# Performance work log

Hardware: AMD Instinct MI355X
Metric: run time of the kernel (lower is better)

The kernel has to match this reference:

```python
import math
import jax, jax.numpy as jnp
import numpy as np

T = 4096
D_MODEL = 1024
NUM_HEADS = 16
HEAD_DIM = D_MODEL // NUM_HEADS


def setup_inputs() -> dict:
    key = jax.random.key(0)
    k_x, k_wqkv, k_wproj = jax.random.split(key, 3)
    # match eqx.nn.Linear init scale: U(-1/sqrt(in), 1/sqrt(in)); randn*small works too,
    # but keep magnitudes reasonable so softmax isn't saturated.
    s_in = 1.0 / math.sqrt(D_MODEL)
    x = jax.random.normal(k_x, (T, D_MODEL), dtype=jnp.float32)
    W_qkv = jax.random.normal(k_wqkv, (3 * D_MODEL, D_MODEL), dtype=jnp.float32) * s_in
    b_qkv = jnp.zeros((3 * D_MODEL,), dtype=jnp.float32)
    W_proj = jax.random.normal(k_wproj, (D_MODEL, D_MODEL), dtype=jnp.float32) * s_in
    b_proj = jnp.zeros((D_MODEL,), dtype=jnp.float32)
    return {"x": x, "W_qkv": W_qkv, "b_qkv": b_qkv, "W_proj": W_proj, "b_proj": b_proj}


def reference(x, W_qkv, b_qkv, W_proj, b_proj):
    T_, C = x.shape  # (seq, d_model)
    H, hd = NUM_HEADS, HEAD_DIM
    # c_attn: eqx Linear computes W @ x + b per token -> x @ W.T + b
    qkv = x @ W_qkv.T + b_qkv  # (T, 3C)
    q, k, v = jnp.split(qkv, 3, axis=1)
    # (T, C) -> (H, T, hd)
    q = q.reshape(T_, H, hd).swapaxes(0, 1)
    k = k.reshape(T_, H, hd).swapaxes(0, 1)
    v = v.reshape(T_, H, hd).swapaxes(0, 1)
    scores = jnp.einsum("htd,hsd->hts", q, k) / math.sqrt(hd)  # (H, T, T)
    causal = jnp.tril(jnp.ones((T_, T_), dtype=bool))
    scores = jnp.where(causal, scores, -jnp.inf)
    attn = jax.nn.softmax(scores, axis=-1)
    y = jnp.einsum("hts,hsd->htd", attn, v)  # (H, T, hd)
    y = y.swapaxes(0, 1).reshape(T_, C)
    y = y @ W_proj.T + b_proj
    return y
```

## Files before the change

kernel.cpp:

```cpp
#include <hip/hip_runtime.h>
#include <math.h>
#include <string.h>

#define T_SEQ 4096
#define DM 1024
#define NH 16
#define HD 64

typedef short s8v __attribute__((ext_vector_type(8)));
typedef float f4v __attribute__((ext_vector_type(4)));

__device__ inline unsigned short f2bf(float f) {
    unsigned u; memcpy(&u, &f, 4);
    u = u + 0x7fffu + ((u >> 16) & 1u);
    return (unsigned short)(u >> 16);
}

__device__ inline float exp2fn(float x) {
#if __has_builtin(__builtin_amdgcn_exp2f)
    return __builtin_amdgcn_exp2f(x);
#else
    return exp2f(x);
#endif
}

__device__ inline void gld_lds16(const void* g, void* l) {
    __builtin_amdgcn_global_load_lds(
        (const __attribute__((address_space(1))) void*)g,
        (__attribute__((address_space(3))) void*)l, 16, 0, 0);
}

__global__ __launch_bounds__(256)
void cvt3(const float* __restrict__ i0, unsigned short* __restrict__ o0, int n0,
          const float* __restrict__ i1, unsigned short* __restrict__ o1, int n1,
          const float* __restrict__ i2, unsigned short* __restrict__ o2, int n2) {
    int i = blockIdx.x * 256 + threadIdx.x;
    const float* in; unsigned short* out; int j;
    if (i < n0)           { in = i0; out = o0; j = i; }
    else if (i < n0 + n1) { in = i1; out = o1; j = i - n0; }
    else if (i < n0 + n1 + n2) { in = i2; out = o2; j = i - n0 - n1; }
    else return;
    const float4* p = (const float4*)(in + (size_t)j * 8);
    float4 a = p[0], b = p[1];
    unsigned short o[8] = {f2bf(a.x), f2bf(a.y), f2bf(a.z), f2bf(a.w),
                           f2bf(b.x), f2bf(b.y), f2bf(b.z), f2bf(b.w)};
    uint4 pk; memcpy(&pk, o, 16);
    *(uint4*)(out + (size_t)j * 8) = pk;
}

template<int MODE, int TN>
__global__ __launch_bounds__(256)
void gemm_bt_mfma(const unsigned short* __restrict__ A, const unsigned short* __restrict__ B,
                  const float* __restrict__ bias, void* __restrict__ Cout,
                  unsigned short* __restrict__ vT,
                  int M, int N, int K) {
    constexpr int NF = TN / 32;
    __shared__ __align__(16) short As[4096];
    __shared__ __align__(16) short Bs[TN * 32];
    const int tid = threadIdx.x;
    const int w = tid >> 6, lane = tid & 63;
    const int wr = w >> 1, wc = w & 1;
    const int m0 = blockIdx.y * 128, n0 = blockIdx.x * TN;

    const bool doA = (w < 2);
    const bool doStage = doA || ((w & 1) * 64 < TN);
    const unsigned short* src = doA ? A : B;
    const int rbase = (doA ? m0 : n0) + (w & 1) * 64;
    const unsigned short* gsrc = src + (size_t)(rbase + (lane & 15)) * K + ((lane >> 4) * 8);
    short* ldst = (doA ? As : Bs) + ((w & 1) * 4) * 512;

    f4v acc[4][NF];
    #pragma unroll
    for (int i = 0; i < 4; ++i)
        #pragma unroll
        for (int j = 0; j < NF; ++j) acc[i][j] = (f4v){0.f, 0.f, 0.f, 0.f};

    for (int k0 = 0; k0 < K; k0 += 32) {
        __syncthreads();
        if (doStage) {
            #pragma unroll
            for (int i = 0; i < 4; ++i)
                gld_lds16(gsrc + (size_t)(i * 16) * K + k0, ldst + i * 512);
        }
        __syncthreads();

        s8v af[4], bf[NF];
        #pragma unroll
        for (int i = 0; i < 4; ++i) af[i] = *(const s8v*)&As[((wr * 4 + i) * 64 + lane) * 8];
        #pragma unroll
        for (int j = 0; j < NF; ++j) bf[j] = *(const s8v*)&Bs[((wc * NF + j) * 64 + lane) * 8];
        #pragma unroll
        for (int i = 0; i < 4; ++i)
            #pragma unroll
            for (int j = 0; j < NF; ++j)
                acc[i][j] = __builtin_amdgcn_mfma_f32_16x16x32_bf16(af[i], bf[j], acc[i][j], 0, 0, 0);
    }

    const int l15 = lane & 15, quad = lane >> 4;
    float bj[NF];
    #pragma unroll
    for (int j = 0; j < NF; ++j) bj[j] = bias[n0 + wc * (TN / 2) + j * 16 + l15];

    if (MODE == 2 && n0 >= 2 * DM) {
        #pragma unroll
        for (int i = 0; i < 4; ++i) {
            int tb = m0 + wr * 64 + i * 16 + quad * 4;
            #pragma unroll
            for (int j = 0; j < NF; ++j) {
                int dg = n0 - 2 * DM + wc * (TN / 2) + j * 16 + l15;
                unsigned short o[4];
                #pragma unroll
                for (int rg = 0; rg < 4; ++rg) o[rg] = f2bf(acc[i][j][rg] + bj[j]);
                unsigned long long pk; memcpy(&pk, o, 8);
                *(unsigned long long*)&vT[(size_t)dg * T_SEQ + tb] = pk;
            }
        }
    } else {
        #pragma unroll
        for (int i = 0; i < 4; ++i) {
            #pragma unroll
            for (int rg = 0; rg < 4; ++rg) {
                int row = m0 + wr * 64 + i * 16 + quad * 4 + rg;
                #pragma unroll
                for (int j = 0; j < NF; ++j) {
                    int col = n0 + wc * (TN / 2) + j * 16 + l15;
                    float v = acc[i][j][rg] + bj[j];
                    if (MODE == 0) ((float*)Cout)[(size_t)row * N + col] = v;
                    else           ((unsigned short*)Cout)[(size_t)row * N + col] = f2bf(v);
                }
            }
        }
    }
}

__device__ __forceinline__ void soft_step(f4v* st, bool diag, int qloc, int quad, int l15,
                                          float& lr, short* pw) {
    const float C2  = 0.1803368851f;
    const float MC2 = 12.0f * 0.1803368851f;
    float sv[4][4];
    #pragma unroll
    for (int kb = 0; kb < 4; ++kb)
        #pragma unroll
        for (int rg = 0; rg < 4; ++rg) {
            float s = st[kb][rg];
            if (diag && (kb * 16 + quad * 4 + rg > qloc)) s = -3.0e38f;
            float t = exp2fn(fmaf(s, C2, -MC2));
            sv[kb][rg] = t;
            lr += t;
        }
    #pragma unroll
    for (int kb = 0; kb < 4; ++kb) {
        unsigned u0 = __float_as_uint(sv[kb][0]) + 0x8000u;
        unsigned u1 = __float_as_uint(sv[kb][1]) + 0x8000u;
        unsigned u2 = __float_as_uint(sv[kb][2]) + 0x8000u;
        unsigned u3 = __float_as_uint(sv[kb][3]) + 0x8000u;
        int2 v;
        v.x = (int)__builtin_amdgcn_perm(u1, u0, 0x07060302);
        v.y = (int)__builtin_amdgcn_perm(u3, u2, 0x07060302);
        int c = (kb >> 1) * 64 + ((kb & 1) * 2 + (quad >> 1)) * 16 + l15;
        c ^= ((c >> 3) & 7);
        *(int2*)&pw[c * 8 + (quad & 1) * 4] = v;
    }
}

__global__ __launch_bounds__(256)
void attn_mfma4(const unsigned short* __restrict__ qkv,
                const unsigned short* __restrict__ vT,
                unsigned short* __restrict__ y) {
    const int b = blockIdx.x;
    const int h = b & 15, a = b >> 4;
    const int tid = threadIdx.x;
    const int w = tid >> 6, lane = tid & 63;
    const int quad = lane >> 4, l15 = lane & 15;
    const int cq = h * HD, hv = h * HD;
    const size_t rs = 3 * DM;

    __shared__ short KB[2][4096];
    __shared__ short VTs[2][4096];
    __shared__ short QB[8192];
    __shared__ short PB[8][1024];

    for (int ph = 0; ph < 2; ++ph) {
        const int qt = ph ? (31 - a) : a;
        const int q0 = qt * 128;
        const int lastk = 2 * qt + 1;

        __syncthreads();
        #pragma unroll
        for (int rr = 0; rr < 4; ++rr) {
            int ch = rr * 256 + tid;
            int qg = ch >> 7, hf = (ch >> 6) & 1, ln = ch & 63;
            gld_lds16(qkv + (size_t)(q0 + qg * 16 + (ln & 15)) * rs + cq + hf * 32 + ((ln >> 4) << 3),
                      &QB[(ch & ~63) * 8]);
        }
        #pragma unroll
        for (int rr = 0; rr < 2; ++rr) {
            int ch = rr * 256 + tid;
            int blk = ch >> 7, hf = (ch >> 6) & 1, ln = ch & 63;
            gld_lds16(qkv + (size_t)(blk * 16 + (ln & 15)) * rs + DM + cq + hf * 32 + ((ln >> 4) << 3),
                      &KB[0][(ch & ~63) * 8]);
            gld_lds16(vT + (size_t)(hv + blk * 16 + (ln & 15)) * T_SEQ + hf * 32 + ((ln >> 4) << 3),
                      &VTs[0][(ch & ~63) * 8]);
        }
        __syncthreads();

        s8v qf[2][2];
        #pragma unroll
        for (int g = 0; g < 2; ++g)
            #pragma unroll
            for (int hf = 0; hf < 2; ++hf)
                qf[g][hf] = *(const s8v*)&QB[((((g * 4 + w) * 2 + hf) * 64) + lane) * 8];

        f4v O0[4], O1[4];
        #pragma unroll
        for (int ob = 0; ob < 4; ++ob) {
            O0[ob] = (f4v){0.f, 0.f, 0.f, 0.f};
            O1[ob] = (f4v){0.f, 0.f, 0.f, 0.f};
        }
        float lr0 = 0.f, lr1 = 0.f;

        for (int kt = 0; kt <= lastk; ++kt) {
            const int p = kt & 1;
            const bool g0a = (kt < lastk);
            if (kt < lastk) {
                const int k1 = (kt + 1) * 64;
                #pragma unroll
                for (int rr = 0; rr < 2; ++rr) {
                    int ch = rr * 256 + tid;
                    int blk = ch >> 7, hf = (ch >> 6) & 1, ln = ch & 63;
                    gld_lds16(qkv + (size_t)(k1 + blk * 16 + (ln & 15)) * rs + DM + cq
                                  + hf * 32 + ((ln >> 4) << 3),
                              &KB[p ^ 1][(ch & ~63) * 8]);
                    gld_lds16(vT + (size_t)(hv + blk * 16 + (ln & 15)) * T_SEQ + k1
                                  + hf * 32 + ((ln >> 4) << 3),
                              &VTs[p ^ 1][(ch & ~63) * 8]);
                }
            }

            f4v st0[4], st1[4];
            #pragma unroll
            for (int kb = 0; kb < 4; ++kb) {
                s8v k0f = *(const s8v*)&KB[p][((kb * 2 + 0) * 64 + lane) * 8];
                s8v k1f = *(const s8v*)&KB[p][((kb * 2 + 1) * 64 + lane) * 8];
                f4v c1 = (f4v){0.f, 0.f, 0.f, 0.f};
                c1 = __builtin_amdgcn_mfma_f32_16x16x32_bf16(k0f, qf[1][0], c1, 0, 0, 0);
                c1 = __builtin_amdgcn_mfma_f32_16x16x32_bf16(k1f, qf[1][1], c1, 0, 0, 0);
                st1[kb] = c1;
                if (g0a) {
                    f4v c0 = (f4v){0.f, 0.f, 0.f, 0.f};
                    c0 = __builtin_amdgcn_mfma_f32_16x16x32_bf16(k0f, qf[0][0], c0, 0, 0, 0);
                    c0 = __builtin_amdgcn_mfma_f32_16x16x32_bf16(k1f, qf[0][1], c0, 0, 0, 0);
                    st0[kb] = c0;
                }
            }

            if (g0a) soft_step(st0, kt == lastk - 1, w * 16 + l15, quad, l15, lr0, PB[w * 2 + 0]);
            soft_step(st1, kt == lastk, w * 16 + l15, quad, l15, lr1, PB[w * 2 + 1]);

            asm volatile("s_waitcnt lgkmcnt(0)" ::: "memory");
            int c0i = lane ^ ((lane >> 3) & 7);
            s8v pf10 = *(const s8v*)&PB[w * 2 + 1][c0i * 8];
            s8v pf11 = *(const s8v*)&PB[w * 2 + 1][(64 + c0i) * 8];
            s8v pf00, pf01;
            if (g0a) {
                pf00 = *(const s8v*)&PB[w * 2 + 0][c0i * 8];
                pf01 = *(const s8v*)&PB[w * 2 + 0][(64 + c0i) * 8];
            }

            #pragma unroll
            for (int ob = 0; ob < 4; ++ob) {
                s8v v0f = *(const s8v*)&VTs[p][((ob * 2 + 0) * 64 + lane) * 8];
                s8v v1f = *(const s8v*)&VTs[p][((ob * 2 + 1) * 64 + lane) * 8];
                O1[ob] = __builtin_amdgcn_mfma_f32_16x16x32_bf16(v0f, pf10, O1[ob], 0, 0, 0);
                O1[ob] = __builtin_amdgcn_mfma_f32_16x16x32_bf16(v1f, pf11, O1[ob], 0, 0, 0);
                if (g0a) {
                    O0[ob] = __builtin_amdgcn_mfma_f32_16x16x32_bf16(v0f, pf00, O0[ob], 0, 0, 0);
                    O0[ob] = __builtin_amdgcn_mfma_f32_16x16x32_bf16(v1f, pf01, O0[ob], 0, 0, 0);
                }
            }
            __syncthreads();
        }

        lr0 += __shfl_xor(lr0, 16); lr0 += __shfl_xor(lr0, 32);
        lr1 += __shfl_xor(lr1, 16); lr1 += __shfl_xor(lr1, 32);
        #pragma unroll
        for (int g = 0; g < 2; ++g) {
            float linv = 1.f / (g ? lr1 : lr0);
            const f4v* O = g ? O1 : O0;
            size_t ybase = (size_t)(q0 + g * 64 + w * 16 + l15) * DM + cq;
            #pragma unroll
            for (int ob = 0; ob < 4; ++ob) {
                unsigned short o[4];
                #pragma unroll
                for (int rg = 0; rg < 4; ++rg) o[rg] = f2bf(O[ob][rg] * linv);
                unsigned long long pk; memcpy(&pk, o, 8);
                *(unsigned long long*)&y[ybase + ob * 16 + quad * 4] = pk;
            }
        }
    }
}

extern "C" void kernel_launch(void* const* d_in, const int* in_sizes, int n_in,
                              void* d_out, int out_size, void* d_ws, size_t ws_size,
                              hipStream_t stream) {
    const float* x     = (const float*)d_in[0];
    const float* Wqkv  = (const float*)d_in[1];
    const float* bqkv  = (const float*)d_in[2];
    const float* Wproj = (const float*)d_in[3];
    const float* bproj = (const float*)d_in[4];
    float* out = (float*)d_out;

    char* ws = (char*)d_ws;
    unsigned short* qkvb  = (unsigned short*)(ws);
    unsigned short* yattb = (unsigned short*)(ws + (24u << 20));
    unsigned short* xb    = (unsigned short*)(ws + (32u << 20));
    unsigned short* wqkvb = (unsigned short*)(ws + (40u << 20));
    unsigned short* wprjb = (unsigned short*)(ws + (46u << 20));
    unsigned short* vTb   = (unsigned short*)(ws + (48u << 20));

    dim3 blk(256);
    {
        int n0 = T_SEQ * DM / 8, n1 = 3 * DM * DM / 8, n2 = DM * DM / 8;
        cvt3<<<dim3((n0 + n1 + n2 + 255) / 256), blk, 0, stream>>>(
            x, xb, n0, Wqkv, wqkvb, n1, Wproj, wprjb, n2);
    }
    gemm_bt_mfma<2, 128><<<dim3(3 * DM / 128, T_SEQ / 128), blk, 0, stream>>>(
        xb, wqkvb, bqkv, qkvb, vTb, T_SEQ, 3 * DM, DM);
    attn_mfma4<<<dim3(NH * 16), blk, 0, stream>>>(qkvb, vTb, yattb);
    gemm_bt_mfma<0, 64><<<dim3(DM / 64, T_SEQ / 128), blk, 0, stream>>>(
        yattb, wprjb, bproj, out, nullptr, T_SEQ, DM, DM);
}
```

Before: 242.1 us.

## Split attention KV range across two blocks and combine partial outputs

Doubles the attention grid from 256 to 512 blocks by assigning even and odd 64-key tiles to separate blocks. Each block writes unnormalized bf16 partial outputs and row sums, and a new combine kernel adds the two partials and normalizes. This targets low occupancy on a GPU with many CUs, where 256 blocks underfill the device. In exchange it adds an extra kernel launch, extra global traffic for two partial buffers, and an extra bf16 rounding of the unnormalized partials. The softmax appears to rely on a fixed max rather than a running one, which is what makes the sum-split valid.

New measurement: 228.7 us. -5.6%, faster.

```diff
diff --git a/kernel.cpp b/kernel.cpp
--- a/kernel.cpp
+++ b/kernel.cpp
@@ -14,6 +14,12 @@
     unsigned u; memcpy(&u, &f, 4);
     u = u + 0x7fffu + ((u >> 16) & 1u);
     return (unsigned short)(u >> 16);
+}
+
+__device__ inline float bf2f(unsigned short s) {
+    unsigned u = (unsigned)s << 16;
+    float f; memcpy(&f, &u, 4);
+    return f;
 }
 
 __device__ inline float exp2fn(float x) {
@@ -163,17 +169,23 @@
     }
 }
 
-__global__ __launch_bounds__(256)
-void attn_mfma4(const unsigned short* __restrict__ qkv,
+__global__ __launch_bounds__(256, 2)
+void attn_mfma5(const unsigned short* __restrict__ qkv,
                 const unsigned short* __restrict__ vT,
-                unsigned short* __restrict__ y) {
+                unsigned short* __restrict__ y0,
+                unsigned short* __restrict__ y1,
+                float* __restrict__ lsum) {
     const int b = blockIdx.x;
-    const int h = b & 15, a = b >> 4;
+    const int par = b & 1;
+    const int idx = b >> 1;
+    const int h = idx & 15, a = idx >> 4;
     const int tid = threadIdx.x;
     const int w = tid >> 6, lane = tid & 63;
     const int quad = lane >> 4, l15 = lane & 15;
     const int cq = h * HD, hv = h * HD;
     const size_t rs = 3 * DM;
+    unsigned short* ypar = par ? y1 : y0;
+    float* lpar = lsum + ((size_t)par * NH + h) * T_SEQ;
 
     __shared__ short KB[2][4096];
     __shared__ short VTs[2][4096];
@@ -183,7 +195,8 @@
     for (int ph = 0; ph < 2; ++ph) {
         const int qt = ph ? (31 - a) : a;
         const int q0 = qt * 128;
-        const int lastk = 2 * qt + 1;
+        const int nk = qt + 1;
+        const int kb0 = par * 64;
 
         __syncthreads();
         #pragma unroll
@@ -197,9 +210,9 @@
         for (int rr = 0; rr < 2; ++rr) {
             int ch = rr * 256 + tid;
             int blk = ch >> 7, hf = (ch >> 6) & 1, ln = ch & 63;
-            gld_lds16(qkv + (size_t)(blk * 16 + (ln & 15)) * rs + DM + cq + hf * 32 + ((ln >> 4) << 3),
+            gld_lds16(qkv + (size_t)(kb0 + blk * 16 + (ln & 15)) * rs + DM + cq + hf * 32 + ((ln >> 4) << 3),
                       &KB[0][(ch & ~63) * 8]);
-            gld_lds16(vT + (size_t)(hv + blk * 16 + (ln & 15)) * T_SEQ + hf * 32 + ((ln >> 4) << 3),
+            gld_lds16(vT + (size_t)(hv + blk * 16 + (ln & 15)) * T_SEQ + kb0 + hf * 32 + ((ln >> 4) << 3),
                       &VTs[0][(ch & ~63) * 8]);
         }
         __syncthreads();
@@ -219,11 +232,14 @@
         }
         float lr0 = 0.f, lr1 = 0.f;
 
-        for (int kt = 0; kt <= lastk; ++kt) {
-            const int p = kt & 1;
-            const bool g0a = (kt < lastk);
-            if (kt < lastk) {
-                const int k1 = (kt + 1) * 64;
+        for (int i = 0; i < nk; ++i) {
+            const int p = i & 1;
+            const bool last = (i == nk - 1);
+            const bool g0a = par ? !last : true;
+            const bool m0 = (par == 0) && last;
+            const bool m1 = (par == 1) && last;
+            if (!last) {
+                const int k1 = kb0 + (i + 1) * 128;
                 #pragma unroll
                 for (int rr = 0; rr < 2; ++rr) {
                     int ch = rr * 256 + tid;
@@ -254,8 +270,8 @@
                 }
             }
 
-            if (g0a) soft_step(st0, kt == lastk - 1, w * 16 + l15, quad, l15, lr0, PB[w * 2 + 0]);
-            soft_step(st1, kt == lastk, w * 16 + l15, quad, l15, lr1, PB[w * 2 + 1]);
+            if (g0a) soft_step(st0, m0, w * 16 + l15, quad, l15, lr0, PB[w * 2 + 0]);
+            soft_step(st1, m1, w * 16 + l15, quad, l15, lr1, PB[w * 2 + 1]);
 
             asm volatile("s_waitcnt lgkmcnt(0)" ::: "memory");
             int c0i = lane ^ ((lane >> 3) & 7);
@@ -285,19 +301,42 @@
         lr1 += __shfl_xor(lr1, 16); lr1 += __shfl_xor(lr1, 32);
         #pragma unroll
         for (int g = 0; g < 2; ++g) {
-            float linv = 1.f / (g ? lr1 : lr0);
             const f4v* O = g ? O1 : O0;
-            size_t ybase = (size_t)(q0 + g * 64 + w * 16 + l15) * DM + cq;
+            int qrow = q0 + g * 64 + w * 16 + l15;
+            size_t ybase = (size_t)qrow * DM + cq;
             #pragma unroll
             for (int ob = 0; ob < 4; ++ob) {
                 unsigned short o[4];
                 #pragma unroll
-                for (int rg = 0; rg < 4; ++rg) o[rg] = f2bf(O[ob][rg] * linv);
+                for (int rg = 0; rg < 4; ++rg) o[rg] = f2bf(O[ob][rg]);
                 unsigned long long pk; memcpy(&pk, o, 8);
-                *(unsigned long long*)&y[ybase + ob * 16 + quad * 4] = pk;
-            }
-        }
-    }
+                *(unsigned long long*)&ypar[ybase + ob * 16 + quad * 4] = pk;
+            }
+            if (quad == 0) lpar[qrow] = g ? lr1 : lr0;
+        }
+    }
+}
+
+__global__ __launch_bounds__(256)
+void attn_combine(const unsigned short* __restrict__ y0,
+                  const unsigned short* __restrict__ y1,
+                  const float* __restrict__ lsum,
+                  unsigned short* __restrict__ yout) {
+    int i = blockIdx.x * 256 + threadIdx.x;
+    int t = i >> 7, d8 = i & 127;
+    int h = d8 >> 3;
+    float l = lsum[(size_t)h * T_SEQ + t] + lsum[((size_t)NH + h) * T_SEQ + t];
+    float inv = 1.f / l;
+    size_t off = (size_t)t * DM + d8 * 8;
+    uint4 ua = *(const uint4*)(y0 + off);
+    uint4 ub = *(const uint4*)(y1 + off);
+    const unsigned short* pa = (const unsigned short*)&ua;
+    const unsigned short* pb = (const unsigned short*)&ub;
+    unsigned short o[8];
+    #pragma unroll
+    for (int k = 0; k < 8; ++k) o[k] = f2bf((bf2f(pa[k]) + bf2f(pb[k])) * inv);
+    uint4 pk; memcpy(&pk, o, 16);
+    *(uint4*)(yout + off) = pk;
 }
 
 extern "C" void kernel_launch(void* const* d_in, const int* in_sizes, int n_in,
@@ -313,10 +352,13 @@
     char* ws = (char*)d_ws;
     unsigned short* qkvb  = (unsigned short*)(ws);
     unsigned short* yattb = (unsigned short*)(ws + (24u << 20));
-    unsigned short* xb    = (unsigned short*)(ws + (32u << 20));
-    unsigned short* wqkvb = (unsigned short*)(ws + (40u << 20));
-    unsigned short* wprjb = (unsigned short*)(ws + (46u << 20));
-    unsigned short* vTb   = (unsigned short*)(ws + (48u << 20));
+    unsigned short* vTb   = (unsigned short*)(ws + (32u << 20));
+    unsigned short* wprjb = (unsigned short*)(ws + (40u << 20));
+    unsigned short* xb    = (unsigned short*)(ws + (42u << 20));
+    unsigned short* wqkvb = (unsigned short*)(ws + (50u << 20));
+    unsigned short* y0p   = (unsigned short*)(ws + (42u << 20));
+    unsigned short* y1p   = (unsigned short*)(ws + (50u << 20));
+    float*          lsum  = (float*)         (ws + (58u << 20));
 
     dim3 blk(256);
     {
@@ -326,7 +368,8 @@
     }
     gemm_bt_mfma<2, 128><<<dim3(3 * DM / 128, T_SEQ / 128), blk, 0, stream>>>(
         xb, wqkvb, bqkv, qkvb, vTb, T_SEQ, 3 * DM, DM);
-    attn_mfma4<<<dim3(NH * 16), blk, 0, stream>>>(qkvb, vTb, yattb);
+    attn_mfma5<<<dim3(512), blk, 0, stream>>>(qkvb, vTb, y0p, y1p, lsum);
+    attn_combine<<<dim3(T_SEQ * DM / 8 / 256), blk, 0, stream>>>(y0p, y1p, lsum, yattb);
     gemm_bt_mfma<0, 64><<<dim3(DM / 64, T_SEQ / 128), blk, 0, stream>>>(
         yattb, wprjb, bproj, out, nullptr, T_SEQ, DM, DM);
 }
```
